# Performance work log

Measured on AMD Instinct MI355X. Metric: run time of the kernel, lower is better.

The kernel has to match this reference:

```python
import jax, jax.numpy as jnp
import numpy as np

B, S, E, H = 1024, 64, 1024, 16  # batch, seq (n_agent+1), n_embd, num_heads
D = E // H  # head_dim = 64


def setup_inputs() -> dict:
    k = jax.random.key(0)
    ks = jax.random.split(k, 7)
    w = lambda i: jax.random.normal(ks[i], (E, E), jnp.float32) * 0.02
    return {
        "query": jax.random.normal(ks[0], (B, S, E), jnp.float32),
        "key": jax.random.normal(ks[1], (B, S, E), jnp.float32),
        "value": jax.random.normal(ks[2], (B, S, E), jnp.float32),
        "Wq": w(3), "bq": jnp.zeros((E,), jnp.float32),
        "Wk": w(4), "bk": jnp.zeros((E,), jnp.float32),
        "Wv": w(5), "bv": jnp.zeros((E,), jnp.float32),
        "Wo": w(6), "bo": jnp.zeros((E,), jnp.float32),
    }


def reference(query, key, value, Wq, bq, Wk, bk, Wv, bv, Wo, bo):
    Bq, Q, _ = query.shape
    K = key.shape[1]
    # projections -> [B, H, L, D]
    q = (query @ Wq + bq).reshape(Bq, Q, H, D).transpose(0, 2, 1, 3)
    k = (key @ Wk + bk).reshape(Bq, K, H, D).transpose(0, 2, 1, 3)
    v = (value @ Wv + bv).reshape(Bq, K, H, D).transpose(0, 2, 1, 3)
    # non-standard: ReLU on Q and K before scores
    q = jnp.maximum(q, 0.0)
    k = jnp.maximum(k, 0.0)
    scale = 1.0 / jnp.sqrt(jnp.float32(D))
    scores = jnp.einsum('bhqd,bhkd->bhqk', q, k) * scale  # [B,H,Q,K]
    # causal mask (tril of the (n_agent+1)^2 mask, sliced to q_len,kv_len)
    mask = jnp.tril(jnp.ones((Q, K), jnp.float32))[None, None]
    scores = jnp.where(mask == 0, jnp.finfo(jnp.float32).min, scores)
    attn = jax.nn.softmax(scores, axis=-1)
    out = jnp.einsum('bhqk,bhkd->bhqd', attn, v)
    out = out.transpose(0, 2, 1, 3).reshape(Bq, Q, E)
    return out @ Wo + bo
```

## Files before the change

### kernel.cpp

```cpp
#include <hip/hip_runtime.h>

typedef __attribute__((ext_vector_type(4))) float f32x4;
typedef __attribute__((ext_vector_type(8))) short short8;
typedef __attribute__((ext_vector_type(2))) unsigned int uint2v;
typedef __attribute__((ext_vector_type(4))) unsigned int uint4v;

#define MFMA_BF16(a,b,c) __builtin_amdgcn_mfma_f32_16x16x32_bf16(a,b,c,0,0,0)

__device__ __forceinline__ unsigned short bf16_of(float f) {
  union { float f; unsigned int u; } v; v.f = f;
  unsigned int r = v.u + 0x7fffu + ((v.u >> 16) & 1u);
  return (unsigned short)(r >> 16);
}

__device__ __forceinline__ unsigned int cvt_pk_bf16(float lo, float hi) {
  unsigned int r;
  asm("v_cvt_pk_bf16_f32 %0, %1, %2" : "=v"(r) : "v"(lo), "v"(hi));
  return r;
}

__device__ __forceinline__ void gload_lds16(const void* g, void* l) {
  __builtin_amdgcn_global_load_lds(
      (const __attribute__((address_space(1))) unsigned int*)g,
      (__attribute__((address_space(3))) unsigned int*)l, 16, 0, 0);
}

__global__ __launch_bounds__(256)
void wcast_kernel(const float* __restrict__ W0, const float* __restrict__ W1,
                  const float* __restrict__ W2, const float* __restrict__ W3,
                  unsigned short* __restrict__ wt) {
  __shared__ float tile[64][65];
  const float* W = (blockIdx.z == 0) ? W0 : (blockIdx.z == 1) ? W1
                 : (blockIdx.z == 2) ? W2 : W3;
  unsigned short* Wt = wt + (size_t)blockIdx.z * (1024u * 1024u);
  int k0 = blockIdx.x * 64, n0 = blockIdx.y * 64;
  int t = threadIdx.x, r = t >> 6, c = t & 63;
#pragma unroll
  for (int i = 0; i < 16; ++i)
    tile[r + i * 4][c] = W[(size_t)(k0 + r + i * 4) * 1024 + n0 + c];
  __syncthreads();
#pragma unroll
  for (int i = 0; i < 16; ++i)
    Wt[(size_t)(n0 + r + i * 4) * 1024 + k0 + c] = bf16_of(tile[c][r + i * 4]);
}

__global__ __launch_bounds__(512, 4)
void gemm_qkv(const float* __restrict__ Aq, const float* __restrict__ Ak,
              const float* __restrict__ Av, const unsigned short* __restrict__ wt,
              const float* __restrict__ bq, const float* __restrict__ bk,
              const float* __restrict__ bv, unsigned short* __restrict__ qw,
              unsigned short* __restrict__ kw, unsigned short* __restrict__ vw) {
  __shared__ unsigned short ldsA[128 * 64];
  __shared__ unsigned short ldsB[256 * 64];

  int z = blockIdx.z;
  const float* Af = (z == 0) ? Aq : (z == 1) ? Ak : Av;
  const unsigned short* Bt = wt + (size_t)z * 1048576;
  const float* bias = (z == 0) ? bq : (z == 1) ? bk : bv;
  unsigned short* C = (z == 0) ? qw : (z == 1) ? kw : vw;

  int bid = blockIdx.x;
  int mt = (bid & 7) * 64 + (bid >> 5);
  int nt = (bid >> 3) & 3;
  int m0 = mt * 128, n0 = nt * 256;

  int tid = threadIdx.x;
  int w = tid >> 6, l = tid & 63;
  int wm = w >> 2, wn = w & 3;
  int li = l & 15, grp = l >> 4;

  f32x4 acc[4][4] = {};

  int grow = l >> 3;
  int gseg = (l & 7) ^ grow;

  int rA = tid >> 2, q = tid & 3;

  f32x4 areg[4];
#pragma unroll
  for (int j = 0; j < 4; ++j)
    areg[j] = *(const f32x4*)(Af + (size_t)(m0 + rA) * 1024 + q * 16 + j * 4);

  for (int kt = 0; kt < 16; ++kt) {
    int k0 = kt * 64;
    {
      uint4v w0, w1;
      w0[0] = cvt_pk_bf16(areg[0][0], areg[0][1]);
      w0[1] = cvt_pk_bf16(areg[0][2], areg[0][3]);
      w0[2] = cvt_pk_bf16(areg[1][0], areg[1][1]);
      w0[3] = cvt_pk_bf16(areg[1][2], areg[1][3]);
      w1[0] = cvt_pk_bf16(areg[2][0], areg[2][1]);
      w1[1] = cvt_pk_bf16(areg[2][2], areg[2][3]);
      w1[2] = cvt_pk_bf16(areg[3][0], areg[3][1]);
      w1[3] = cvt_pk_bf16(areg[3][2], areg[3][3]);
      *(uint4v*)((char*)ldsA + rA * 128 + (((2 * q)     ^ (rA & 7)) << 4)) = w0;
      *(uint4v*)((char*)ldsA + rA * 128 + (((2 * q + 1) ^ (rA & 7)) << 4)) = w1;
    }
#pragma unroll
    for (int i = 0; i < 4; ++i) {
      int c = w * 4 + i;
      gload_lds16(Bt + (size_t)(n0 + 8 * c + grow) * 1024 + k0 + gseg * 8,
                  (char*)ldsB + c * 1024);
    }
    if (kt < 15) {
#pragma unroll
      for (int j = 0; j < 4; ++j)
        areg[j] = *(const f32x4*)(Af + (size_t)(m0 + rA) * 1024 + (k0 + 64) + q * 16 + j * 4);
    }
    __syncthreads();
#pragma unroll
    for (int ks = 0; ks < 2; ++ks) {
      short8 af[4], bf[4];
#pragma unroll
      for (int mi = 0; mi < 4; ++mi) {
        int row = wm * 64 + mi * 16 + li;
        af[mi] = *(const short8*)((const char*)ldsA + row * 128 +
                                  (((ks * 4 + grp) ^ (row & 7)) << 4));
      }
#pragma unroll
      for (int ni = 0; ni < 4; ++ni) {
        int row = wn * 64 + ni * 16 + li;
        bf[ni] = *(const short8*)((const char*)ldsB + row * 128 +
                                  (((ks * 4 + grp) ^ (row & 7)) << 4));
      }
#pragma unroll
      for (int mi = 0; mi < 4; ++mi)
#pragma unroll
        for (int ni = 0; ni < 4; ++ni)
          acc[mi][ni] = MFMA_BF16(af[mi], bf[ni], acc[mi][ni]);
    }
    __syncthreads();
  }

  int mrow0 = m0 + wm * 64;
  int ncol0 = n0 + wn * 64;
  float bvv[4];
#pragma unroll
  for (int ni = 0; ni < 4; ++ni) bvv[ni] = bias[ncol0 + ni * 16 + li];

  int b = mrow0 >> 6, h = ncol0 >> 6;
  unsigned short* base = C + (size_t)b * 65536 + (size_t)h * 4096;
  if (z < 2) {
#pragma unroll
    for (int mi = 0; mi < 4; ++mi)
#pragma unroll
      for (int ni = 0; ni < 4; ++ni)
#pragma unroll
        for (int j = 0; j < 4; ++j) {
          float v = acc[mi][ni][j] + bvv[ni];
          v = fmaxf(v, 0.0f);
          base[(mi * 16 + grp * 4 + j) * 64 + ni * 16 + li] = bf16_of(v);
        }
  } else {
#pragma unroll
    for (int mi = 0; mi < 4; ++mi)
#pragma unroll
      for (int ni = 0; ni < 4; ++ni) {
        uint2v pk;
        pk.x = cvt_pk_bf16(acc[mi][ni][0] + bvv[ni], acc[mi][ni][1] + bvv[ni]);
        pk.y = cvt_pk_bf16(acc[mi][ni][2] + bvv[ni], acc[mi][ni][3] + bvv[ni]);
        *(uint2v*)(base + (ni * 16 + li) * 64 + mi * 16 + grp * 4) = pk;
      }
  }
}

__global__ __launch_bounds__(256, 4)
void gemm_out(const unsigned short* __restrict__ Ab, const unsigned short* __restrict__ Bt,
              const float* __restrict__ bias, float* __restrict__ C) {
  __shared__ unsigned short ldsA[2][128 * 64];
  __shared__ unsigned short ldsB[2][128 * 64];

  int bid = blockIdx.x;
  int mt = (bid & 7) * 64 + (bid >> 6);
  int nt = (bid >> 3) & 7;
  int m0 = mt * 128, n0 = nt * 128;

  int tid = threadIdx.x;
  int w = tid >> 6, l = tid & 63;
  int wm = w >> 1, wn = w & 1;
  int li = l & 15, grp = l >> 4;

  f32x4 acc[4][4] = {};

  int grow = l >> 3;
  int gseg = (l & 7) ^ grow;

  auto stage = [&](int buf, int kt) {
#pragma unroll
    for (int i = 0; i < 4; ++i) {
      int c = w * 4 + i;
      gload_lds16(Ab + (size_t)(m0 + 8 * c + grow) * 1024 + kt * 64 + gseg * 8,
                  (char*)&ldsA[buf][0] + c * 1024);
    }
#pragma unroll
    for (int i = 0; i < 4; ++i) {
      int c = w * 4 + i;
      gload_lds16(Bt + (size_t)(n0 + 8 * c + grow) * 1024 + kt * 64 + gseg * 8,
                  (char*)&ldsB[buf][0] + c * 1024);
    }
  };

  stage(0, 0);
  __syncthreads();

  for (int kt = 0; kt < 16; ++kt) {
    int cur = kt & 1;
    if (kt < 15) {
      stage(cur ^ 1, kt + 1);
      __builtin_amdgcn_sched_barrier(0);
    }
#pragma unroll
    for (int ks = 0; ks < 2; ++ks) {
      short8 af[4], bf[4];
#pragma unroll
      for (int mi = 0; mi < 4; ++mi) {
        int row = wm * 64 + mi * 16 + li;
        af[mi] = *(const short8*)((const char*)&ldsA[cur][0] + row * 128 +
                                  (((ks * 4 + grp) ^ (row & 7)) << 4));
      }
#pragma unroll
      for (int ni = 0; ni < 4; ++ni) {
        int row = wn * 64 + ni * 16 + li;
        bf[ni] = *(const short8*)((const char*)&ldsB[cur][0] + row * 128 +
                                  (((ks * 4 + grp) ^ (row & 7)) << 4));
      }
#pragma unroll
      for (int mi = 0; mi < 4; ++mi)
#pragma unroll
        for (int ni = 0; ni < 4; ++ni)
          acc[mi][ni] = MFMA_BF16(af[mi], bf[ni], acc[mi][ni]);
    }
    __syncthreads();
  }

  int mrow0 = m0 + wm * 64;
  int ncol0 = n0 + wn * 64;
  float bvv[4];
#pragma unroll
  for (int ni = 0; ni < 4; ++ni) bvv[ni] = bias[ncol0 + ni * 16 + li];
#pragma unroll
  for (int mi = 0; mi < 4; ++mi)
#pragma unroll
    for (int ni = 0; ni < 4; ++ni)
#pragma unroll
      for (int j = 0; j < 4; ++j)
        C[(size_t)(mrow0 + mi * 16 + grp * 4 + j) * 1024 + ncol0 + ni * 16 + li] =
            acc[mi][ni][j] + bvv[ni];
}

__global__ __launch_bounds__(64)
void attn_kernel(const unsigned short* __restrict__ qw,
                 const unsigned short* __restrict__ kw,
                 const unsigned short* __restrict__ vw,
                 unsigned short* __restrict__ aw) {
  __shared__ unsigned short p_lds[64 * 72];
  int bh = blockIdx.x;
  int b = bh >> 4, h = bh & 15;
  int l = threadIdx.x;
  int li = l & 15, grp = l >> 4;
  const unsigned short* qb = qw + (size_t)bh * 4096;
  const unsigned short* kb = kw + (size_t)bh * 4096;
  const unsigned short* vb = vw + (size_t)bh * 4096;

  short8 aq[4][2], bk_[4][2];
#pragma unroll
  for (int mi = 0; mi < 4; ++mi)
#pragma unroll
    for (int ks = 0; ks < 2; ++ks) {
      aq[mi][ks]  = *(const short8*)(qb + (mi * 16 + li) * 64 + ks * 32 + grp * 8);
      bk_[mi][ks] = *(const short8*)(kb + (mi * 16 + li) * 64 + ks * 32 + grp * 8);
    }

  f32x4 sf[4][4];
#pragma unroll
  for (int mi = 0; mi < 4; ++mi)
#pragma unroll
    for (int ni = 0; ni < 4; ++ni) {
      f32x4 t = {};
      t = MFMA_BF16(aq[mi][0], bk_[ni][0], t);
      t = MFMA_BF16(aq[mi][1], bk_[ni][1], t);
      sf[mi][ni] = t;
    }

#pragma unroll
  for (int mi = 0; mi < 4; ++mi) {
#pragma unroll
    for (int j = 0; j < 4; ++j) {
      int row = mi * 16 + grp * 4 + j;
      float mx = -1e30f;
#pragma unroll
      for (int ni = 0; ni < 4; ++ni) {
        int col = ni * 16 + li;
        float v = sf[mi][ni][j] * 0.125f;
        v = (col <= row) ? v : -1e30f;
        sf[mi][ni][j] = v;
        mx = fmaxf(mx, v);
      }
#pragma unroll
      for (int sh = 1; sh < 16; sh <<= 1) mx = fmaxf(mx, __shfl_xor(mx, sh, 64));
      float sum = 0.0f;
#pragma unroll
      for (int ni = 0; ni < 4; ++ni) {
        float e = __expf(sf[mi][ni][j] - mx);
        sf[mi][ni][j] = e;
        sum += e;
      }
#pragma unroll
      for (int sh = 1; sh < 16; sh <<= 1) sum += __shfl_xor(sum, sh, 64);
      float rr = 1.0f / sum;
#pragma unroll
      for (int ni = 0; ni < 4; ++ni) sf[mi][ni][j] *= rr;
    }
  }

#pragma unroll
  for (int mi = 0; mi < 4; ++mi)
#pragma unroll
    for (int ni = 0; ni < 4; ++ni)
#pragma unroll
      for (int j = 0; j < 4; ++j)
        p_lds[(mi * 16 + grp * 4 + j) * 72 + ni * 16 + li] = bf16_of(sf[mi][ni][j]);
  __syncthreads();

  short8 pa[4][2], bv_[4][2];
#pragma unroll
  for (int mi = 0; mi < 4; ++mi)
#pragma unroll
    for (int ks = 0; ks < 2; ++ks)
      pa[mi][ks] = *(const short8*)(p_lds + (mi * 16 + li) * 72 + ks * 32 + grp * 8);
#pragma unroll
  for (int ni = 0; ni < 4; ++ni)
#pragma unroll
    for (int ks = 0; ks < 2; ++ks)
      bv_[ni][ks] = *(const short8*)(vb + (ni * 16 + li) * 64 + ks * 32 + grp * 8);

  f32x4 of[4][4];
#pragma unroll
  for (int mi = 0; mi < 4; ++mi)
#pragma unroll
    for (int ni = 0; ni < 4; ++ni) {
      f32x4 t = {};
      t = MFMA_BF16(pa[mi][0], bv_[ni][0], t);
      t = MFMA_BF16(pa[mi][1], bv_[ni][1], t);
      of[mi][ni] = t;
    }

  unsigned short* ab = aw + (size_t)b * 65536 + (size_t)h * 64;
#pragma unroll
  for (int mi = 0; mi < 4; ++mi)
#pragma unroll
    for (int ni = 0; ni < 4; ++ni)
#pragma unroll
      for (int j = 0; j < 4; ++j)
        ab[(size_t)(mi * 16 + grp * 4 + j) * 1024 + ni * 16 + li] = bf16_of(of[mi][ni][j]);
}

extern "C" void kernel_launch(void* const* d_in, const int* in_sizes, int n_in,
                              void* d_out, int out_size, void* d_ws, size_t ws_size,
                              hipStream_t stream) {
  (void)in_sizes; (void)n_in; (void)out_size; (void)ws_size;
  const float* query = (const float*)d_in[0];
  const float* key   = (const float*)d_in[1];
  const float* value = (const float*)d_in[2];
  const float* Wq = (const float*)d_in[3];
  const float* bq = (const float*)d_in[4];
  const float* Wk = (const float*)d_in[5];
  const float* bk = (const float*)d_in[6];
  const float* Wv = (const float*)d_in[7];
  const float* bv = (const float*)d_in[8];
  const float* Wo = (const float*)d_in[9];
  const float* bo = (const float*)d_in[10];
  float* out = (float*)d_out;

  unsigned short* wt = (unsigned short*)d_ws;
  const size_t NE = (size_t)67108864;
  unsigned short* qw = wt + (size_t)4 * 1024 * 1024;
  unsigned short* kw = qw + NE;
  unsigned short* vw = kw + NE;
  unsigned short* aw = vw + NE;

  wcast_kernel<<<dim3(16, 16, 4), 256, 0, stream>>>(Wq, Wk, Wv, Wo, wt);
  gemm_qkv<<<dim3(2048, 1, 3), 512, 0, stream>>>(query, key, value, wt,
                                                 bq, bk, bv, qw, kw, vw);
  attn_kernel<<<dim3(16384), 64, 0, stream>>>(qw, kw, vw, aw);
  gemm_out<<<dim3(4096), 256, 0, stream>>>(aw, wt + (size_t)3 * 1048576, bo, out);
}
```

Baseline: 968.3 us.

## Multi-buffer QKV GEMM pipeline and retile output GEMM to 128x256 blocks

The QKV projection GEMM gains a software pipeline. B tiles are triple-buffered in LDS through async global-to-LDS loads, A tiles are double-buffered in registers and LDS, and explicit vmcnt waits let loads run two k-steps ahead instead of stalling on one buffer. The output GEMM is retiled to match, moving from 256-thread 128x128 double-buffered blocks to 512-thread 128x256 single-buffered blocks. This raises LDS use and cuts occupancy for gemm_qkv (launch bounds drop to 2 blocks). It also removes the prefetch overlap in gemm_out, trading that for larger tiles with more reuse.

```diff
diff --git a/kernel.cpp b/kernel.cpp
--- a/kernel.cpp
+++ b/kernel.cpp
@@ -44,14 +44,14 @@
     Wt[(size_t)(n0 + r + i * 4) * 1024 + k0 + c] = bf16_of(tile[c][r + i * 4]);
 }
 
-__global__ __launch_bounds__(512, 4)
+__global__ __launch_bounds__(512, 2)
 void gemm_qkv(const float* __restrict__ Aq, const float* __restrict__ Ak,
               const float* __restrict__ Av, const unsigned short* __restrict__ wt,
               const float* __restrict__ bq, const float* __restrict__ bk,
               const float* __restrict__ bv, unsigned short* __restrict__ qw,
               unsigned short* __restrict__ kw, unsigned short* __restrict__ vw) {
-  __shared__ unsigned short ldsA[128 * 64];
-  __shared__ unsigned short ldsB[256 * 64];
+  __shared__ unsigned short ldsA[2][128 * 64];
+  __shared__ unsigned short ldsB[3][256 * 64];
 
   int z = blockIdx.z;
   const float* Af = (z == 0) ? Aq : (z == 1) ? Ak : Av;
@@ -73,54 +73,67 @@
 
   int grow = l >> 3;
   int gseg = (l & 7) ^ grow;
-
   int rA = tid >> 2, q = tid & 3;
 
-  f32x4 areg[4];
-#pragma unroll
-  for (int j = 0; j < 4; ++j)
-    areg[j] = *(const f32x4*)(Af + (size_t)(m0 + rA) * 1024 + q * 16 + j * 4);
-
-  for (int kt = 0; kt < 16; ++kt) {
-    int k0 = kt * 64;
-    {
-      uint4v w0, w1;
-      w0[0] = cvt_pk_bf16(areg[0][0], areg[0][1]);
-      w0[1] = cvt_pk_bf16(areg[0][2], areg[0][3]);
-      w0[2] = cvt_pk_bf16(areg[1][0], areg[1][1]);
-      w0[3] = cvt_pk_bf16(areg[1][2], areg[1][3]);
-      w1[0] = cvt_pk_bf16(areg[2][0], areg[2][1]);
-      w1[1] = cvt_pk_bf16(areg[2][2], areg[2][3]);
-      w1[2] = cvt_pk_bf16(areg[3][0], areg[3][1]);
-      w1[3] = cvt_pk_bf16(areg[3][2], areg[3][3]);
-      *(uint4v*)((char*)ldsA + rA * 128 + (((2 * q)     ^ (rA & 7)) << 4)) = w0;
-      *(uint4v*)((char*)ldsA + rA * 128 + (((2 * q + 1) ^ (rA & 7)) << 4)) = w1;
-    }
+  auto stageB = [&](int buf, int kt) {
 #pragma unroll
     for (int i = 0; i < 4; ++i) {
       int c = w * 4 + i;
-      gload_lds16(Bt + (size_t)(n0 + 8 * c + grow) * 1024 + k0 + gseg * 8,
-                  (char*)ldsB + c * 1024);
-    }
-    if (kt < 15) {
-#pragma unroll
-      for (int j = 0; j < 4; ++j)
-        areg[j] = *(const f32x4*)(Af + (size_t)(m0 + rA) * 1024 + (k0 + 64) + q * 16 + j * 4);
-    }
-    __syncthreads();
+      gload_lds16(Bt + (size_t)(n0 + 8 * c + grow) * 1024 + kt * 64 + gseg * 8,
+                  (char*)&ldsB[buf][0] + c * 1024);
+    }
+  };
+  auto loadA = [&](f32x4* ar, int kt) {
+#pragma unroll
+    for (int j = 0; j < 4; ++j)
+      ar[j] = *(const f32x4*)(Af + (size_t)(m0 + rA) * 1024 + kt * 64 + q * 16 + j * 4);
+  };
+  auto writeA = [&](const f32x4* ar, int buf) {
+    uint4v w0, w1;
+    w0[0] = cvt_pk_bf16(ar[0][0], ar[0][1]);
+    w0[1] = cvt_pk_bf16(ar[0][2], ar[0][3]);
+    w0[2] = cvt_pk_bf16(ar[1][0], ar[1][1]);
+    w0[3] = cvt_pk_bf16(ar[1][2], ar[1][3]);
+    w1[0] = cvt_pk_bf16(ar[2][0], ar[2][1]);
+    w1[1] = cvt_pk_bf16(ar[2][2], ar[2][3]);
+    w1[2] = cvt_pk_bf16(ar[3][0], ar[3][1]);
+    w1[3] = cvt_pk_bf16(ar[3][2], ar[3][3]);
+    *(uint4v*)((char*)&ldsA[buf][0] + rA * 128 + (((2 * q)     ^ (rA & 7)) << 4)) = w0;
+    *(uint4v*)((char*)&ldsA[buf][0] + rA * 128 + (((2 * q + 1) ^ (rA & 7)) << 4)) = w1;
+  };
+
+  f32x4 ax[4], ay[4];
+
+  stageB(0, 0); loadA(ax, 0);
+  __builtin_amdgcn_sched_barrier(0);
+  stageB(1, 1); loadA(ay, 1);
+  __builtin_amdgcn_sched_barrier(0);
+  asm volatile("s_waitcnt vmcnt(8)" ::: "memory");
+  writeA(ax, 0);
+  asm volatile("s_waitcnt lgkmcnt(0)" ::: "memory");
+  __builtin_amdgcn_s_barrier();
+  __builtin_amdgcn_sched_barrier(0);
+
+#pragma unroll
+  for (int t = 0; t < 16; ++t) {
+    if (t <= 13) {
+      stageB((t + 2) % 3, t + 2);
+      if ((t & 1) == 0) loadA(ax, t + 2); else loadA(ay, t + 2);
+      __builtin_amdgcn_sched_barrier(0);
+    }
 #pragma unroll
     for (int ks = 0; ks < 2; ++ks) {
       short8 af[4], bf[4];
 #pragma unroll
       for (int mi = 0; mi < 4; ++mi) {
         int row = wm * 64 + mi * 16 + li;
-        af[mi] = *(const short8*)((const char*)ldsA + row * 128 +
+        af[mi] = *(const short8*)((const char*)&ldsA[t & 1][0] + row * 128 +
                                   (((ks * 4 + grp) ^ (row & 7)) << 4));
       }
 #pragma unroll
       for (int ni = 0; ni < 4; ++ni) {
         int row = wn * 64 + ni * 16 + li;
-        bf[ni] = *(const short8*)((const char*)ldsB + row * 128 +
+        bf[ni] = *(const short8*)((const char*)&ldsB[t % 3][0] + row * 128 +
                                   (((ks * 4 + grp) ^ (row & 7)) << 4));
       }
 #pragma unroll
@@ -129,7 +142,14 @@
         for (int ni = 0; ni < 4; ++ni)
           acc[mi][ni] = MFMA_BF16(af[mi], bf[ni], acc[mi][ni]);
     }
-    __syncthreads();
+    if (t <= 14) {
+      if (t <= 13) asm volatile("s_waitcnt vmcnt(8)" ::: "memory");
+      else         asm volatile("s_waitcnt vmcnt(0)" ::: "memory");
+      if ((t & 1) == 0) writeA(ay, 1); else writeA(ax, 0);
+      asm volatile("s_waitcnt lgkmcnt(0)" ::: "memory");
+      __builtin_amdgcn_s_barrier();
+      __builtin_amdgcn_sched_barrier(0);
+    }
   }
 
   int mrow0 = m0 + wm * 64;
@@ -164,20 +184,20 @@
   }
 }
 
-__global__ __launch_bounds__(256, 4)
+__global__ __launch_bounds__(512, 4)
 void gemm_out(const unsigned short* __restrict__ Ab, const unsigned short* __restrict__ Bt,
               const float* __restrict__ bias, float* __restrict__ C) {
-  __shared__ unsigned short ldsA[2][128 * 64];
-  __shared__ unsigned short ldsB[2][128 * 64];
+  __shared__ unsigned short ldsA[128 * 64];
+  __shared__ unsigned short ldsB[256 * 64];
 
   int bid = blockIdx.x;
-  int mt = (bid & 7) * 64 + (bid >> 6);
-  int nt = (bid >> 3) & 7;
-  int m0 = mt * 128, n0 = nt * 128;
+  int mt = (bid & 7) * 64 + (bid >> 5);
+  int nt = (bid >> 3) & 3;
+  int m0 = mt * 128, n0 = nt * 256;
 
   int tid = threadIdx.x;
   int w = tid >> 6, l = tid & 63;
-  int wm = w >> 1, wn = w & 1;
+  int wm = w >> 2, wn = w & 3;
   int li = l & 15, grp = l >> 4;
 
   f32x4 acc[4][4] = {};
@@ -185,43 +205,34 @@
   int grow = l >> 3;
   int gseg = (l & 7) ^ grow;
 
-  auto stage = [&](int buf, int kt) {
+  for (int kt = 0; kt < 16; ++kt) {
+    int k0 = kt * 64;
+#pragma unroll
+    for (int i = 0; i < 2; ++i) {
+      int c = w * 2 + i;
+      gload_lds16(Ab + (size_t)(m0 + 8 * c + grow) * 1024 + k0 + gseg * 8,
+                  (char*)ldsA + c * 1024);
+    }
 #pragma unroll
     for (int i = 0; i < 4; ++i) {
       int c = w * 4 + i;
-      gload_lds16(Ab + (size_t)(m0 + 8 * c + grow) * 1024 + kt * 64 + gseg * 8,
-                  (char*)&ldsA[buf][0] + c * 1024);
-    }
-#pragma unroll
-    for (int i = 0; i < 4; ++i) {
-      int c = w * 4 + i;
-      gload_lds16(Bt + (size_t)(n0 + 8 * c + grow) * 1024 + kt * 64 + gseg * 8,
-                  (char*)&ldsB[buf][0] + c * 1024);
-    }
-  };
-
-  stage(0, 0);
-  __syncthreads();
-
-  for (int kt = 0; kt < 16; ++kt) {
-    int cur = kt & 1;
-    if (kt < 15) {
-      stage(cur ^ 1, kt + 1);
-      __builtin_amdgcn_sched_barrier(0);
-    }
+      gload_lds16(Bt + (size_t)(n0 + 8 * c + grow) * 1024 + k0 + gseg * 8,
+                  (char*)ldsB + c * 1024);
+    }
+    __syncthreads();
 #pragma unroll
     for (int ks = 0; ks < 2; ++ks) {
       short8 af[4], bf[4];
 #pragma unroll
       for (int mi = 0; mi < 4; ++mi) {
         int row = wm * 64 + mi * 16 + li;
-        af[mi] = *(const short8*)((const char*)&ldsA[cur][0] + row * 128 +
+        af[mi] = *(const short8*)((const char*)ldsA + row * 128 +
                                   (((ks * 4 + grp) ^ (row & 7)) << 4));
       }
 #pragma unroll
       for (int ni = 0; ni < 4; ++ni) {
         int row = wn * 64 + ni * 16 + li;
-        bf[ni] = *(const short8*)((const char*)&ldsB[cur][0] + row * 128 +
+        bf[ni] = *(const short8*)((const char*)ldsB + row * 128 +
                                   (((ks * 4 + grp) ^ (row & 7)) << 4));
       }
 #pragma unroll
@@ -383,5 +394,5 @@
   gemm_qkv<<<dim3(2048, 1, 3), 512, 0, stream>>>(query, key, value, wt,
                                                  bq, bk, bv, qw, kw, vw);
   attn_kernel<<<dim3(16384), 64, 0, stream>>>(qw, kw, vw, aw);
-  gemm_out<<<dim3(4096), 256, 0, stream>>>(aw, wt + (size_t)3 * 1048576, bo, out);
-}
+  gemm_out<<<dim3(2048), 512, 0, stream>>>(aw, wt + (size_t)3 * 1048576, bo, out);
+}
```

Measured after the change: 1.082 ms. 11.7% more time.

## Shrink QKV GEMM tile to 128x128 and single-buffer output GEMM LDS

Applied to the files above, without the earlier changes.

The QKV projection GEMM moves from 512-thread blocks with 128x256 tiles to 256-thread blocks with 128x128 tiles, doubling the grid. Each thread now loads and converts twice as many fp32 A values per k-step, as 8 vectors. The output GEMM drops its double-buffered LDS staging and loads each k-tile synchronously before computing. This halves LDS use per block, which may allow more resident blocks, but it gives up weight reuse per tile and the overlap of loads with MFMA work.

```diff
diff --git a/kernel.cpp b/kernel.cpp
--- a/kernel.cpp
+++ b/kernel.cpp
@@ -44,14 +44,14 @@
     Wt[(size_t)(n0 + r + i * 4) * 1024 + k0 + c] = bf16_of(tile[c][r + i * 4]);
 }
 
-__global__ __launch_bounds__(512, 4)
+__global__ __launch_bounds__(256, 4)
 void gemm_qkv(const float* __restrict__ Aq, const float* __restrict__ Ak,
               const float* __restrict__ Av, const unsigned short* __restrict__ wt,
               const float* __restrict__ bq, const float* __restrict__ bk,
               const float* __restrict__ bv, unsigned short* __restrict__ qw,
               unsigned short* __restrict__ kw, unsigned short* __restrict__ vw) {
   __shared__ unsigned short ldsA[128 * 64];
-  __shared__ unsigned short ldsB[256 * 64];
+  __shared__ unsigned short ldsB[128 * 64];
 
   int z = blockIdx.z;
   const float* Af = (z == 0) ? Aq : (z == 1) ? Ak : Av;
@@ -60,13 +60,13 @@
   unsigned short* C = (z == 0) ? qw : (z == 1) ? kw : vw;
 
   int bid = blockIdx.x;
-  int mt = (bid & 7) * 64 + (bid >> 5);
-  int nt = (bid >> 3) & 3;
-  int m0 = mt * 128, n0 = nt * 256;
+  int mt = (bid & 7) * 64 + (bid >> 6);
+  int nt = (bid >> 3) & 7;
+  int m0 = mt * 128, n0 = nt * 128;
 
   int tid = threadIdx.x;
   int w = tid >> 6, l = tid & 63;
-  int wm = w >> 2, wn = w & 3;
+  int wm = w >> 1, wn = w & 1;
   int li = l & 15, grp = l >> 4;
 
   f32x4 acc[4][4] = {};
@@ -74,39 +74,38 @@
   int grow = l >> 3;
   int gseg = (l & 7) ^ grow;
 
-  int rA = tid >> 2, q = tid & 3;
-
-  f32x4 areg[4];
-#pragma unroll
-  for (int j = 0; j < 4; ++j)
-    areg[j] = *(const f32x4*)(Af + (size_t)(m0 + rA) * 1024 + q * 16 + j * 4);
+  int rA = tid >> 1, q = tid & 1;
+
+  f32x4 areg[8];
+  auto loadA = [&](int kt) {
+#pragma unroll
+    for (int j = 0; j < 8; ++j)
+      areg[j] = *(const f32x4*)(Af + (size_t)(m0 + rA) * 1024 + kt * 64 + q * 32 + j * 4);
+  };
+  auto writeA = [&]() {
+#pragma unroll
+    for (int p = 0; p < 4; ++p) {
+      uint4v wv;
+      wv[0] = cvt_pk_bf16(areg[2 * p][0], areg[2 * p][1]);
+      wv[1] = cvt_pk_bf16(areg[2 * p][2], areg[2 * p][3]);
+      wv[2] = cvt_pk_bf16(areg[2 * p + 1][0], areg[2 * p + 1][1]);
+      wv[3] = cvt_pk_bf16(areg[2 * p + 1][2], areg[2 * p + 1][3]);
+      *(uint4v*)((char*)ldsA + rA * 128 + (((4 * q + p) ^ (rA & 7)) << 4)) = wv;
+    }
+  };
+
+  loadA(0);
 
   for (int kt = 0; kt < 16; ++kt) {
     int k0 = kt * 64;
-    {
-      uint4v w0, w1;
-      w0[0] = cvt_pk_bf16(areg[0][0], areg[0][1]);
-      w0[1] = cvt_pk_bf16(areg[0][2], areg[0][3]);
-      w0[2] = cvt_pk_bf16(areg[1][0], areg[1][1]);
-      w0[3] = cvt_pk_bf16(areg[1][2], areg[1][3]);
-      w1[0] = cvt_pk_bf16(areg[2][0], areg[2][1]);
-      w1[1] = cvt_pk_bf16(areg[2][2], areg[2][3]);
-      w1[2] = cvt_pk_bf16(areg[3][0], areg[3][1]);
-      w1[3] = cvt_pk_bf16(areg[3][2], areg[3][3]);
-      *(uint4v*)((char*)ldsA + rA * 128 + (((2 * q)     ^ (rA & 7)) << 4)) = w0;
-      *(uint4v*)((char*)ldsA + rA * 128 + (((2 * q + 1) ^ (rA & 7)) << 4)) = w1;
-    }
+    writeA();
 #pragma unroll
     for (int i = 0; i < 4; ++i) {
       int c = w * 4 + i;
       gload_lds16(Bt + (size_t)(n0 + 8 * c + grow) * 1024 + k0 + gseg * 8,
                   (char*)ldsB + c * 1024);
     }
-    if (kt < 15) {
-#pragma unroll
-      for (int j = 0; j < 4; ++j)
-        areg[j] = *(const f32x4*)(Af + (size_t)(m0 + rA) * 1024 + (k0 + 64) + q * 16 + j * 4);
-    }
+    if (kt < 15) loadA(kt + 1);
     __syncthreads();
 #pragma unroll
     for (int ks = 0; ks < 2; ++ks) {
@@ -167,8 +166,8 @@
 __global__ __launch_bounds__(256, 4)
 void gemm_out(const unsigned short* __restrict__ Ab, const unsigned short* __restrict__ Bt,
               const float* __restrict__ bias, float* __restrict__ C) {
-  __shared__ unsigned short ldsA[2][128 * 64];
-  __shared__ unsigned short ldsB[2][128 * 64];
+  __shared__ unsigned short ldsA[128 * 64];
+  __shared__ unsigned short ldsB[128 * 64];
 
   int bid = blockIdx.x;
   int mt = (bid & 7) * 64 + (bid >> 6);
@@ -185,43 +184,34 @@
   int grow = l >> 3;
   int gseg = (l & 7) ^ grow;
 
-  auto stage = [&](int buf, int kt) {
+  for (int kt = 0; kt < 16; ++kt) {
+    int k0 = kt * 64;
 #pragma unroll
     for (int i = 0; i < 4; ++i) {
       int c = w * 4 + i;
-      gload_lds16(Ab + (size_t)(m0 + 8 * c + grow) * 1024 + kt * 64 + gseg * 8,
-                  (char*)&ldsA[buf][0] + c * 1024);
+      gload_lds16(Ab + (size_t)(m0 + 8 * c + grow) * 1024 + k0 + gseg * 8,
+                  (char*)ldsA + c * 1024);
     }
 #pragma unroll
     for (int i = 0; i < 4; ++i) {
       int c = w * 4 + i;
-      gload_lds16(Bt + (size_t)(n0 + 8 * c + grow) * 1024 + kt * 64 + gseg * 8,
-                  (char*)&ldsB[buf][0] + c * 1024);
-    }
-  };
-
-  stage(0, 0);
-  __syncthreads();
-
-  for (int kt = 0; kt < 16; ++kt) {
-    int cur = kt & 1;
-    if (kt < 15) {
-      stage(cur ^ 1, kt + 1);
-      __builtin_amdgcn_sched_barrier(0);
-    }
+      gload_lds16(Bt + (size_t)(n0 + 8 * c + grow) * 1024 + k0 + gseg * 8,
+                  (char*)ldsB + c * 1024);
+    }
+    __syncthreads();
 #pragma unroll
     for (int ks = 0; ks < 2; ++ks) {
       short8 af[4], bf[4];
 #pragma unroll
       for (int mi = 0; mi < 4; ++mi) {
         int row = wm * 64 + mi * 16 + li;
-        af[mi] = *(const short8*)((const char*)&ldsA[cur][0] + row * 128 +
+        af[mi] = *(const short8*)((const char*)ldsA + row * 128 +
                                   (((ks * 4 + grp) ^ (row & 7)) << 4));
       }
 #pragma unroll
       for (int ni = 0; ni < 4; ++ni) {
         int row = wn * 64 + ni * 16 + li;
-        bf[ni] = *(const short8*)((const char*)&ldsB[cur][0] + row * 128 +
+        bf[ni] = *(const short8*)((const char*)ldsB + row * 128 +
                                   (((ks * 4 + grp) ^ (row & 7)) << 4));
       }
 #pragma unroll
@@ -380,7 +370,7 @@
   unsigned short* aw = vw + NE;
 
   wcast_kernel<<<dim3(16, 16, 4), 256, 0, stream>>>(Wq, Wk, Wv, Wo, wt);
-  gemm_qkv<<<dim3(2048, 1, 3), 512, 0, stream>>>(query, key, value, wt,
+  gemm_qkv<<<dim3(4096, 1, 3), 256, 0, stream>>>(query, key, value, wt,
                                                  bq, bk, bv, qw, kw, vw);
   attn_kernel<<<dim3(16384), 64, 0, stream>>>(qw, kw, vw, aw);
   gemm_out<<<dim3(4096), 256, 0, stream>>>(aw, wt + (size_t)3 * 1048576, bo, out);
```

New measurement: 1.693 ms. 1.75x slower.

## Retile output GEMM to 128x256 with 512 threads, single-buffered LDS

Applied to the files above, without the earlier changes.

The output projection GEMM moves from 128x128 tiles with 256 threads and double-buffered LDS to 128x256 tiles with 512 threads and a single LDS buffer, matching the QKV GEMM structure. The larger tile is meant to raise reuse of the A operand and halve the block count, at the cost of losing the prefetch overlap the double buffer provided. In the QKV GEMM, the register prefetch of the next A tile now happens after the barrier, with a scheduling barrier so the global loads are issued ahead of the MFMA work.

```diff
diff --git a/kernel.cpp b/kernel.cpp
--- a/kernel.cpp
+++ b/kernel.cpp
@@ -77,9 +77,13 @@
   int rA = tid >> 2, q = tid & 3;
 
   f32x4 areg[4];
-#pragma unroll
-  for (int j = 0; j < 4; ++j)
-    areg[j] = *(const f32x4*)(Af + (size_t)(m0 + rA) * 1024 + q * 16 + j * 4);
+  auto loadA = [&](int kt) {
+#pragma unroll
+    for (int j = 0; j < 4; ++j)
+      areg[j] = *(const f32x4*)(Af + (size_t)(m0 + rA) * 1024 + kt * 64 + q * 16 + j * 4);
+  };
+
+  loadA(0);
 
   for (int kt = 0; kt < 16; ++kt) {
     int k0 = kt * 64;
@@ -102,12 +106,11 @@
       gload_lds16(Bt + (size_t)(n0 + 8 * c + grow) * 1024 + k0 + gseg * 8,
                   (char*)ldsB + c * 1024);
     }
+    __syncthreads();
     if (kt < 15) {
-#pragma unroll
-      for (int j = 0; j < 4; ++j)
-        areg[j] = *(const f32x4*)(Af + (size_t)(m0 + rA) * 1024 + (k0 + 64) + q * 16 + j * 4);
-    }
-    __syncthreads();
+      loadA(kt + 1);
+      __builtin_amdgcn_sched_barrier(0);
+    }
 #pragma unroll
     for (int ks = 0; ks < 2; ++ks) {
       short8 af[4], bf[4];
@@ -164,20 +167,20 @@
   }
 }
 
-__global__ __launch_bounds__(256, 4)
+__global__ __launch_bounds__(512, 4)
 void gemm_out(const unsigned short* __restrict__ Ab, const unsigned short* __restrict__ Bt,
               const float* __restrict__ bias, float* __restrict__ C) {
-  __shared__ unsigned short ldsA[2][128 * 64];
-  __shared__ unsigned short ldsB[2][128 * 64];
+  __shared__ unsigned short ldsA[128 * 64];
+  __shared__ unsigned short ldsB[256 * 64];
 
   int bid = blockIdx.x;
-  int mt = (bid & 7) * 64 + (bid >> 6);
-  int nt = (bid >> 3) & 7;
-  int m0 = mt * 128, n0 = nt * 128;
+  int mt = (bid & 7) * 64 + (bid >> 5);
+  int nt = (bid >> 3) & 3;
+  int m0 = mt * 128, n0 = nt * 256;
 
   int tid = threadIdx.x;
   int w = tid >> 6, l = tid & 63;
-  int wm = w >> 1, wn = w & 1;
+  int wm = w >> 2, wn = w & 3;
   int li = l & 15, grp = l >> 4;
 
   f32x4 acc[4][4] = {};
@@ -185,43 +188,34 @@
   int grow = l >> 3;
   int gseg = (l & 7) ^ grow;
 
-  auto stage = [&](int buf, int kt) {
+  for (int kt = 0; kt < 16; ++kt) {
+    int k0 = kt * 64;
+#pragma unroll
+    for (int i = 0; i < 2; ++i) {
+      int c = w * 2 + i;
+      gload_lds16(Ab + (size_t)(m0 + 8 * c + grow) * 1024 + k0 + gseg * 8,
+                  (char*)ldsA + c * 1024);
+    }
 #pragma unroll
     for (int i = 0; i < 4; ++i) {
       int c = w * 4 + i;
-      gload_lds16(Ab + (size_t)(m0 + 8 * c + grow) * 1024 + kt * 64 + gseg * 8,
-                  (char*)&ldsA[buf][0] + c * 1024);
-    }
-#pragma unroll
-    for (int i = 0; i < 4; ++i) {
-      int c = w * 4 + i;
-      gload_lds16(Bt + (size_t)(n0 + 8 * c + grow) * 1024 + kt * 64 + gseg * 8,
-                  (char*)&ldsB[buf][0] + c * 1024);
-    }
-  };
-
-  stage(0, 0);
-  __syncthreads();
-
-  for (int kt = 0; kt < 16; ++kt) {
-    int cur = kt & 1;
-    if (kt < 15) {
-      stage(cur ^ 1, kt + 1);
-      __builtin_amdgcn_sched_barrier(0);
-    }
+      gload_lds16(Bt + (size_t)(n0 + 8 * c + grow) * 1024 + k0 + gseg * 8,
+                  (char*)ldsB + c * 1024);
+    }
+    __syncthreads();
 #pragma unroll
     for (int ks = 0; ks < 2; ++ks) {
       short8 af[4], bf[4];
 #pragma unroll
       for (int mi = 0; mi < 4; ++mi) {
         int row = wm * 64 + mi * 16 + li;
-        af[mi] = *(const short8*)((const char*)&ldsA[cur][0] + row * 128 +
+        af[mi] = *(const short8*)((const char*)ldsA + row * 128 +
                                   (((ks * 4 + grp) ^ (row & 7)) << 4));
       }
 #pragma unroll
       for (int ni = 0; ni < 4; ++ni) {
         int row = wn * 64 + ni * 16 + li;
-        bf[ni] = *(const short8*)((const char*)&ldsB[cur][0] + row * 128 +
+        bf[ni] = *(const short8*)((const char*)ldsB + row * 128 +
                                   (((ks * 4 + grp) ^ (row & 7)) << 4));
       }
 #pragma unroll
@@ -383,5 +377,5 @@
   gemm_qkv<<<dim3(2048, 1, 3), 512, 0, stream>>>(query, key, value, wt,
                                                  bq, bk, bv, qw, kw, vw);
   attn_kernel<<<dim3(16384), 64, 0, stream>>>(qw, kw, vw, aw);
-  gemm_out<<<dim3(4096), 256, 0, stream>>>(aw, wt + (size_t)3 * 1048576, bo, out);
-}
+  gemm_out<<<dim3(2048), 512, 0, stream>>>(aw, wt + (size_t)3 * 1048576, bo, out);
+}
```

Result: faster. 830.0 us (-14.3%).
